# Kernel tuning notes

Hardware: AMD Instinct MI355X
Metric: run time of the kernel (lower is better)

## Reference

```python
import jax, jax.numpy as jnp
import numpy as np

V, H, E, O = 50257, 256, 256, 64
T, B = 1024, 256


def setup_inputs() -> dict:
    key = jax.random.key(0)
    ks = jax.random.split(key, 10)
    s = 0.02
    return {
        "x": jax.random.randint(ks[0], (T, B), 0, V, dtype=jnp.int64),
        "emb": jax.random.normal(ks[1], (V, H), jnp.float32) * s,
        "W_i2h": jax.random.normal(ks[2], (H, 2 * H), jnp.float32) * s,
        "b_i2h": jnp.zeros((H,), jnp.float32),
        "W_i2o": jax.random.normal(ks[3], (H, 2 * H), jnp.float32) * s,
        "b_i2o": jnp.zeros((H,), jnp.float32),
        "W_o2o": jax.random.normal(ks[4], (E, 2 * H), jnp.float32) * s,
        "b_o2o": jnp.zeros((E,), jnp.float32),
        "W_pred": jax.random.normal(ks[5], (O, E), jnp.float32) * s,
        "b_pred": jnp.zeros((O,), jnp.float32),
    }


def reference(x, emb, W_i2h, b_i2h, W_i2o, b_i2o, W_o2o, b_o2o, W_pred, b_pred):
    Bsz = x.shape[1]

    def step(h, xt):
        e = emb[xt]                                   # [B, H]
        ic = jnp.concatenate([e, h], axis=1)          # [B, 2H]
        h_new = ic @ W_i2h.T + b_i2h                  # [B, H]
        o = ic @ W_i2o.T + b_i2o                      # [B, H]
        oc = jnp.concatenate([h_new, o], axis=1)      # [B, 2H]
        out = oc @ W_o2o.T + b_o2o                    # [B, E]
        return h_new, out

    h0 = jnp.zeros((Bsz, W_i2h.shape[0]), emb.dtype)
    _, outs = jax.lax.scan(step, h0, x)               # [T, B, E]
    encoded = jnp.mean(outs, axis=0)                  # mean over time (dropout = identity in eval)
    logits = encoded @ W_pred.T + b_pred              # [B, O]
    logprobs = jax.nn.log_softmax(logits, axis=1)
    preds = jnp.argmax(logprobs, axis=1)
    probs = jnp.exp(logprobs)
    return preds, logprobs, probs
```

## Files before the change

kernel.cpp:

```cpp
#include <hip/hip_runtime.h>

#define T_STEPS 1024
#define BSZ 256
#define HD 256
#define OUTC 64
#define NT 32
#define NPHASE 32
#define TBB 8
#define BT 16

static const size_t OFF_SUM  = 0;
static const size_t OFF_FLAG = 65536;
static const size_t OFF_WP   = 65600;
static const size_t OFF_CEH  = 458816;
static const size_t OFF_CEO  = 2555968;
static const size_t OFF_H    = 4653120;
static const size_t OFF_A2   = 6815808;

__global__ void detect_x(const int* __restrict__ x, float* __restrict__ ws) {
    __shared__ int nonzero;
    if (threadIdx.x == 0) nonzero = 0;
    __syncthreads();
    if (x[2 * threadIdx.x + 1] != 0) nonzero = 1;
    __syncthreads();
    if (threadIdx.x == 0) *(int*)(ws + OFF_FLAG) = (nonzero == 0) ? 1 : 0;
}

__global__ void prep_pack(const float* __restrict__ Wi2h,
                          const float* __restrict__ Wi2o,
                          const float* __restrict__ Wo2o,
                          float* __restrict__ ws) {
    const int q = blockIdx.x;
    const int z = blockIdx.y;
    const int j = threadIdx.x;
    const float* src = (z == 0) ? Wi2h : (z == 1) ? Wi2o : Wo2o;
    const float4 v = *reinterpret_cast<const float4*>(src + (size_t)j * 512 + 4 * q);
    reinterpret_cast<float4*>(ws + OFF_WP)[((size_t)z * 128 + q) * 256 + j] = v;
}

__device__ __forceinline__ float RLf(float v, int l) {
    return __int_as_float(__builtin_amdgcn_readlane(__float_as_int(v), l));
}

__global__ __launch_bounds__(256) void kernB(
    const int* __restrict__ x, const float* __restrict__ emb,
    const float* __restrict__ boo, float* __restrict__ ws, int phase) {
    const int tid = threadIdx.x;
    const int sg = tid >> 7;
    const int lj = tid & 127;
    const int j0 = lj, j1 = lj + 128;
    const int ti = blockIdx.x;
    const int row = blockIdx.y;
    const int mode64 = *(const int*)(ws + OFF_FLAG);
    const float4* __restrict__ Wh4  = reinterpret_cast<const float4*>(ws + OFF_WP);
    const float4* __restrict__ Wio4 = Wh4 + (size_t)128 * 256;

    if (ti == 0 && phase > 0) {
        const size_t rb = (size_t)row * 256 + tid;
        float av[NT];
        #pragma unroll
        for (int i = 0; i < NT; ++i)
            av[i] = ws[OFF_A2 + (size_t)i * 65536 + rb];
        float s = (phase == 1) ? 0.f : ws[OFF_SUM + rb];
        const float boo_j = boo[tid];
        #pragma unroll
        for (int i = 0; i < NT; ++i) s += (av[i] + boo_j);
        ws[OFF_SUM + rb] = s;
    }

    __shared__ int toks[BT];
    __shared__ __align__(16) float eW[BT][256];
    if (tid < BT) {
        const int t = phase * NT + ti * BT + tid;
        toks[tid] = mode64 ? x[2 * (t * BSZ + row)] : x[t * BSZ + row];
    }
    __syncthreads();
    #pragma unroll
    for (int v = 0; v < BT; ++v)
        eW[v][tid] = emb[(size_t)toks[v] * HD + tid];
    __syncthreads();

    float aH[TBB][2], aO[TBB][2];
    #pragma unroll
    for (int u = 0; u < TBB; ++u) {
        aH[u][0] = 0.f; aH[u][1] = 0.f; aO[u][0] = 0.f; aO[u][1] = 0.f;
    }
    #pragma unroll 2
    for (int q = 0; q < 64; ++q) {
        const float4 whA = Wh4[(size_t)q * 256 + j0];
        const float4 whB = Wh4[(size_t)q * 256 + j1];
        const float4 woA = Wio4[(size_t)q * 256 + j0];
        const float4 woB = Wio4[(size_t)q * 256 + j1];
        #pragma unroll
        for (int u = 0; u < TBB; ++u) {
            const float4 e = *reinterpret_cast<const float4*>(&eW[sg * TBB + u][4 * q]);
            aH[u][0] = fmaf(e.x, whA.x, aH[u][0]); aH[u][1] = fmaf(e.x, whB.x, aH[u][1]);
            aO[u][0] = fmaf(e.x, woA.x, aO[u][0]); aO[u][1] = fmaf(e.x, woB.x, aO[u][1]);
            aH[u][0] = fmaf(e.y, whA.y, aH[u][0]); aH[u][1] = fmaf(e.y, whB.y, aH[u][1]);
            aO[u][0] = fmaf(e.y, woA.y, aO[u][0]); aO[u][1] = fmaf(e.y, woB.y, aO[u][1]);
            aH[u][0] = fmaf(e.z, whA.z, aH[u][0]); aH[u][1] = fmaf(e.z, whB.z, aH[u][1]);
            aO[u][0] = fmaf(e.z, woA.z, aO[u][0]); aO[u][1] = fmaf(e.z, woB.z, aO[u][1]);
            aH[u][0] = fmaf(e.w, whA.w, aH[u][0]); aH[u][1] = fmaf(e.w, whB.w, aH[u][1]);
            aO[u][0] = fmaf(e.w, woA.w, aO[u][0]); aO[u][1] = fmaf(e.w, woB.w, aO[u][1]);
        }
    }
    const size_t rb = (size_t)row * 256;
    #pragma unroll
    for (int u = 0; u < TBB; ++u) {
        const size_t off = (size_t)(ti * BT + sg * TBB + u) * 65536 + rb;
        ws[OFF_CEH + off + j0] = aH[u][0];
        ws[OFF_CEH + off + j1] = aH[u][1];
        ws[OFF_CEO + off + j0] = aO[u][0];
        ws[OFF_CEO + off + j1] = aO[u][1];
    }
}

__global__ __launch_bounds__(256) void kernC(
    const float* __restrict__ bih, float* __restrict__ ws, int phase) {
    const int j = threadIdx.x;
    const int lane = j & 63;
    const int row = blockIdx.x;
    const float4* __restrict__ Wh4 = reinterpret_cast<const float4*>(ws + OFF_WP);

    float4 whr[64];
    #pragma unroll
    for (int q = 0; q < 64; ++q) whr[q] = Wh4[(size_t)(64 + q) * 256 + j];

    __shared__ __align__(16) float hCur[256];
    float* __restrict__ Hp = ws + OFF_H;
    const float* __restrict__ CE = ws + OFF_CEH;
    const size_t rb = (size_t)row * 256 + j;

    const float hc = (phase == 0) ? 0.f : Hp[(size_t)NT * 65536 + rb];
    Hp[rb] = hc;
    hCur[j] = hc;
    const float bih_j = bih[j];
    float ceCur = CE[rb];
    __syncthreads();

    #pragma unroll 1
    for (int i = 0; i < NT; ++i) {
        const float ceNext = (i + 1 < NT) ? CE[(size_t)(i + 1) * 65536 + rb] : 0.f;
        const float4 h4 = *reinterpret_cast<const float4*>(&hCur[4 * lane]);
        float ah = ceCur;
        #pragma unroll
        for (int p2 = 0; p2 < 32; ++p2) {
            const int q0 = 2 * p2, q1 = 2 * p2 + 1;
            const float4 a = *reinterpret_cast<const float4*>(&hCur[4 * q0]);
            ah = fmaf(a.x, whr[q0].x, ah);
            ah = fmaf(a.y, whr[q0].y, ah);
            ah = fmaf(a.z, whr[q0].z, ah);
            ah = fmaf(a.w, whr[q0].w, ah);
            ah = fmaf(RLf(h4.x, q1), whr[q1].x, ah);
            ah = fmaf(RLf(h4.y, q1), whr[q1].y, ah);
            ah = fmaf(RLf(h4.z, q1), whr[q1].z, ah);
            ah = fmaf(RLf(h4.w, q1), whr[q1].w, ah);
        }
        const float hn = ah + bih_j;
        Hp[(size_t)(i + 1) * 65536 + rb] = hn;
        __syncthreads();
        hCur[j] = hn;
        ceCur = ceNext;
        __syncthreads();
    }
}

__global__ __launch_bounds__(256) void kernD(
    const float* __restrict__ bio, float* __restrict__ ws, int phase) {
    const int tid = threadIdx.x;
    const int sg = tid >> 7;
    const int lj = tid & 127;
    const int j0 = lj, j1 = lj + 128;
    const int ti = blockIdx.x;
    const int row = blockIdx.y;
    const float4* __restrict__ Wh4  = reinterpret_cast<const float4*>(ws + OFF_WP);
    const float4* __restrict__ Wio4 = Wh4 + (size_t)128 * 256;
    const float4* __restrict__ Woo4 = Wh4 + (size_t)256 * 256;

    __shared__ __align__(16) float hS[BT + 1][256];
    __shared__ __align__(16) float oS[BT][256];
    const float* __restrict__ Hp = ws + OFF_H;
    const size_t rb = (size_t)row * 256;

    #pragma unroll
    for (int v = 0; v <= BT; ++v)
        hS[v][tid] = Hp[(size_t)(ti * BT + v) * 65536 + rb + tid];
    float co[TBB][2], a2[TBB][2];
    #pragma unroll
    for (int u = 0; u < TBB; ++u) {
        const size_t off = OFF_CEO + (size_t)(ti * BT + sg * TBB + u) * 65536 + rb;
        co[u][0] = ws[off + j0];
        co[u][1] = ws[off + j1];
        a2[u][0] = 0.f; a2[u][1] = 0.f;
    }
    __syncthreads();

    #pragma unroll 2
    for (int q = 0; q < 64; ++q) {
        const float4 w1A = Wio4[(size_t)(64 + q) * 256 + j0];
        const float4 w1B = Wio4[(size_t)(64 + q) * 256 + j1];
        const float4 w2A = Woo4[(size_t)q * 256 + j0];
        const float4 w2B = Woo4[(size_t)q * 256 + j1];
        float4 hq[TBB + 1];
        #pragma unroll
        for (int v = 0; v <= TBB; ++v)
            hq[v] = *reinterpret_cast<const float4*>(&hS[sg * TBB + v][4 * q]);
        #pragma unroll
        for (int u = 0; u < TBB; ++u) {
            co[u][0] = fmaf(hq[u].x, w1A.x, co[u][0]);
            co[u][1] = fmaf(hq[u].x, w1B.x, co[u][1]);
            co[u][0] = fmaf(hq[u].y, w1A.y, co[u][0]);
            co[u][1] = fmaf(hq[u].y, w1B.y, co[u][1]);
            co[u][0] = fmaf(hq[u].z, w1A.z, co[u][0]);
            co[u][1] = fmaf(hq[u].z, w1B.z, co[u][1]);
            co[u][0] = fmaf(hq[u].w, w1A.w, co[u][0]);
            co[u][1] = fmaf(hq[u].w, w1B.w, co[u][1]);
            a2[u][0] = fmaf(hq[u + 1].x, w2A.x, a2[u][0]);
            a2[u][1] = fmaf(hq[u + 1].x, w2B.x, a2[u][1]);
            a2[u][0] = fmaf(hq[u + 1].y, w2A.y, a2[u][0]);
            a2[u][1] = fmaf(hq[u + 1].y, w2B.y, a2[u][1]);
            a2[u][0] = fmaf(hq[u + 1].z, w2A.z, a2[u][0]);
            a2[u][1] = fmaf(hq[u + 1].z, w2B.z, a2[u][1]);
            a2[u][0] = fmaf(hq[u + 1].w, w2A.w, a2[u][0]);
            a2[u][1] = fmaf(hq[u + 1].w, w2B.w, a2[u][1]);
        }
    }
    const float bio_j0 = bio[j0], bio_j1 = bio[j1];
    #pragma unroll
    for (int u = 0; u < TBB; ++u) {
        oS[sg * TBB + u][j0] = co[u][0] + bio_j0;
        oS[sg * TBB + u][j1] = co[u][1] + bio_j1;
    }
    __syncthreads();

    #pragma unroll 2
    for (int q = 0; q < 64; ++q) {
        const float4 w3A = Woo4[(size_t)(64 + q) * 256 + j0];
        const float4 w3B = Woo4[(size_t)(64 + q) * 256 + j1];
        #pragma unroll
        for (int u = 0; u < TBB; ++u) {
            const float4 o4 = *reinterpret_cast<const float4*>(&oS[sg * TBB + u][4 * q]);
            a2[u][0] = fmaf(o4.x, w3A.x, a2[u][0]);
            a2[u][1] = fmaf(o4.x, w3B.x, a2[u][1]);
            a2[u][0] = fmaf(o4.y, w3A.y, a2[u][0]);
            a2[u][1] = fmaf(o4.y, w3B.y, a2[u][1]);
            a2[u][0] = fmaf(o4.z, w3A.z, a2[u][0]);
            a2[u][1] = fmaf(o4.z, w3B.z, a2[u][1]);
            a2[u][0] = fmaf(o4.w, w3A.w, a2[u][0]);
            a2[u][1] = fmaf(o4.w, w3B.w, a2[u][1]);
        }
    }
    #pragma unroll
    for (int u = 0; u < TBB; ++u) {
        const size_t off = OFF_A2 + (size_t)(ti * BT + sg * TBB + u) * 65536 + rb;
        ws[off + j0] = a2[u][0];
        ws[off + j1] = a2[u][1];
    }
}

__global__ __launch_bounds__(64) void final_k(
    const float* __restrict__ Wpred, const float* __restrict__ bpred,
    const float* __restrict__ boo, const float* __restrict__ ws,
    float* __restrict__ out) {
    const int b = blockIdx.x, o = threadIdx.x;
    __shared__ float enc[256];
    __shared__ float exs[64];
    __shared__ float s32s;

    #pragma unroll
    for (int u = 0; u < 4; ++u) {
        const int j = o * 4 + u;
        const size_t rb = (size_t)b * 256 + j;
        float av[NT];
        #pragma unroll
        for (int i = 0; i < NT; ++i)
            av[i] = ws[OFF_A2 + (size_t)i * 65536 + rb];
        float s = ws[OFF_SUM + rb];
        const float boo_j = boo[j];
        #pragma unroll
        for (int i = 0; i < NT; ++i) s += (av[i] + boo_j);
        enc[j] = s * (1.0f / 1024.0f);
    }
    __syncthreads();

    float acc = 0.f;
    for (int e = 0; e < 256; ++e)
        acc = fmaf(enc[e], Wpred[(size_t)o * 256 + e], acc);
    acc += bpred[o];

    float m = acc;
    #pragma unroll
    for (int d = 1; d < 64; d <<= 1) m = fmaxf(m, __shfl_xor(m, d));
    const float sh = acc - m;
    const float ex = (float)exp((double)sh);
    exs[o] = ex;
    __syncthreads();
    if (o == 0) {
        double sd = 0.0;
        for (int i = 0; i < 64; ++i) sd += (double)exs[i];
        s32s = (float)sd;
    }
    __syncthreads();
    const float log_s = (float)log((double)s32s);
    const float lp = sh - log_s;
    const float pr = (float)exp((double)lp);

    float av = lp; int ai = o;
    #pragma unroll
    for (int d = 1; d < 64; d <<= 1) {
        const float ov = __shfl_xor(av, d);
        const int oi = __shfl_xor(ai, d);
        if (ov > av || (ov == av && oi < ai)) { av = ov; ai = oi; }
    }

    out[BSZ + (size_t)b * OUTC + o] = lp;
    out[BSZ + 16384 + (size_t)b * OUTC + o] = pr;
    if (o == 0) out[b] = (float)ai;
}

extern "C" void kernel_launch(void* const* d_in, const int* in_sizes, int n_in,
                              void* d_out, int out_size, void* d_ws, size_t ws_size,
                              hipStream_t stream) {
    const int*   x     = (const int*)d_in[0];
    const float* emb   = (const float*)d_in[1];
    const float* Wi2h  = (const float*)d_in[2];
    const float* b_ih  = (const float*)d_in[3];
    const float* Wi2o  = (const float*)d_in[4];
    const float* b_io  = (const float*)d_in[5];
    const float* Wo2o  = (const float*)d_in[6];
    const float* b_oo  = (const float*)d_in[7];
    const float* Wpred = (const float*)d_in[8];
    const float* b_p   = (const float*)d_in[9];
    float* ws  = (float*)d_ws;
    float* out = (float*)d_out;

    detect_x<<<1, 256, 0, stream>>>(x, ws);
    prep_pack<<<dim3(128, 3), 256, 0, stream>>>(Wi2h, Wi2o, Wo2o, ws);

    for (int p = 0; p < NPHASE; ++p) {
        kernB<<<dim3(2, 256), 256, 0, stream>>>(x, emb, b_oo, ws, p);
        kernC<<<dim3(256), 256, 0, stream>>>(b_ih, ws, p);
        kernD<<<dim3(2, 256), 256, 0, stream>>>(b_io, ws, p);
    }
    final_k<<<dim3(256), 64, 0, stream>>>(Wpred, b_p, b_oo, ws, out);
}
```

Measured before the change: 5.599 ms.

## Process two batch rows per recurrence block, streaming weights from global

The sequential hidden-state recurrence kernel now handles two batch rows per block, which halves the grid to 128 blocks. The 64-float4 register-resident weight slice is replaced by a software-prefetched stream from global/L2, with each weight load reused for both rows. Ping-pong shared buffers drop one of the two barriers per step. This frees a large amount of registers and reuses weights, but each serial step now does twice the FMA work plus repeated global weight loads, which may lengthen the critical path of the recurrence.

```diff
diff --git a/kernel.cpp b/kernel.cpp
--- a/kernel.cpp
+++ b/kernel.cpp
@@ -119,48 +119,56 @@
     const float* __restrict__ bih, float* __restrict__ ws, int phase) {
     const int j = threadIdx.x;
     const int lane = j & 63;
-    const int row = blockIdx.x;
+    const int r0 = blockIdx.x * 2, r1 = r0 + 1;
     const float4* __restrict__ Wh4 = reinterpret_cast<const float4*>(ws + OFF_WP);
 
-    float4 whr[64];
-    #pragma unroll
-    for (int q = 0; q < 64; ++q) whr[q] = Wh4[(size_t)(64 + q) * 256 + j];
-
-    __shared__ __align__(16) float hCur[256];
+    __shared__ __align__(16) float h0Ping[256], h0Pong[256];
+    __shared__ __align__(16) float h1Ping[256], h1Pong[256];
     float* __restrict__ Hp = ws + OFF_H;
     const float* __restrict__ CE = ws + OFF_CEH;
-    const size_t rb = (size_t)row * 256 + j;
-
-    const float hc = (phase == 0) ? 0.f : Hp[(size_t)NT * 65536 + rb];
-    Hp[rb] = hc;
-    hCur[j] = hc;
+    const size_t rb0 = (size_t)r0 * 256 + j;
+    const size_t rb1 = (size_t)r1 * 256 + j;
+
+    const float hc0 = (phase == 0) ? 0.f : Hp[(size_t)NT * 65536 + rb0];
+    const float hc1 = (phase == 0) ? 0.f : Hp[(size_t)NT * 65536 + rb1];
+    Hp[rb0] = hc0; Hp[rb1] = hc1;
+    h0Ping[j] = hc0; h1Ping[j] = hc1;
     const float bih_j = bih[j];
-    float ceCur = CE[rb];
+    float ce0 = CE[rb0], ce1 = CE[rb1];
     __syncthreads();
 
     #pragma unroll 1
     for (int i = 0; i < NT; ++i) {
-        const float ceNext = (i + 1 < NT) ? CE[(size_t)(i + 1) * 65536 + rb] : 0.f;
-        const float4 h4 = *reinterpret_cast<const float4*>(&hCur[4 * lane]);
-        float ah = ceCur;
-        #pragma unroll
-        for (int p2 = 0; p2 < 32; ++p2) {
-            const int q0 = 2 * p2, q1 = 2 * p2 + 1;
-            const float4 a = *reinterpret_cast<const float4*>(&hCur[4 * q0]);
-            ah = fmaf(a.x, whr[q0].x, ah);
-            ah = fmaf(a.y, whr[q0].y, ah);
-            ah = fmaf(a.z, whr[q0].z, ah);
-            ah = fmaf(a.w, whr[q0].w, ah);
-            ah = fmaf(RLf(h4.x, q1), whr[q1].x, ah);
-            ah = fmaf(RLf(h4.y, q1), whr[q1].y, ah);
-            ah = fmaf(RLf(h4.z, q1), whr[q1].z, ah);
-            ah = fmaf(RLf(h4.w, q1), whr[q1].w, ah);
+        const float ce0n = (i + 1 < NT) ? CE[(size_t)(i + 1) * 65536 + rb0] : 0.f;
+        const float ce1n = (i + 1 < NT) ? CE[(size_t)(i + 1) * 65536 + rb1] : 0.f;
+        const float* __restrict__ hb0 = (i & 1) ? h0Pong : h0Ping;
+        const float* __restrict__ hb1 = (i & 1) ? h1Pong : h1Ping;
+        float* __restrict__ hn0      = (i & 1) ? h0Ping : h0Pong;
+        float* __restrict__ hn1      = (i & 1) ? h1Ping : h1Pong;
+        const float4 h4r1 = *reinterpret_cast<const float4*>(&hb1[4 * lane]);
+        float ah0 = ce0, ah1 = ce1;
+        float4 w = Wh4[(size_t)64 * 256 + j];
+        #pragma unroll 4
+        for (int q = 0; q < 64; ++q) {
+            const float4 wn = Wh4[(size_t)(64 + ((q + 1) & 63)) * 256 + j];
+            const float4 a = *reinterpret_cast<const float4*>(&hb0[4 * q]);
+            ah0 = fmaf(a.x, w.x, ah0);
+            ah0 = fmaf(a.y, w.y, ah0);
+            ah0 = fmaf(a.z, w.z, ah0);
+            ah0 = fmaf(a.w, w.w, ah0);
+            float s;
+            s = RLf(h4r1.x, q); ah1 = fmaf(s, w.x, ah1);
+            s = RLf(h4r1.y, q); ah1 = fmaf(s, w.y, ah1);
+            s = RLf(h4r1.z, q); ah1 = fmaf(s, w.z, ah1);
+            s = RLf(h4r1.w, q); ah1 = fmaf(s, w.w, ah1);
+            w = wn;
         }
-        const float hn = ah + bih_j;
-        Hp[(size_t)(i + 1) * 65536 + rb] = hn;
-        __syncthreads();
-        hCur[j] = hn;
-        ceCur = ceNext;
+        const float hv0 = ah0 + bih_j;
+        const float hv1 = ah1 + bih_j;
+        Hp[(size_t)(i + 1) * 65536 + rb0] = hv0;
+        Hp[(size_t)(i + 1) * 65536 + rb1] = hv1;
+        hn0[j] = hv0; hn1[j] = hv1;
+        ce0 = ce0n; ce1 = ce1n;
         __syncthreads();
     }
 }
@@ -339,7 +347,7 @@
 
     for (int p = 0; p < NPHASE; ++p) {
         kernB<<<dim3(2, 256), 256, 0, stream>>>(x, emb, b_oo, ws, p);
-        kernC<<<dim3(256), 256, 0, stream>>>(b_ih, ws, p);
+        kernC<<<dim3(128), 256, 0, stream>>>(b_ih, ws, p);
         kernD<<<dim3(2, 256), 256, 0, stream>>>(b_io, ws, p);
     }
     final_k<<<dim3(256), 64, 0, stream>>>(Wpred, b_p, b_oo, ws, out);
```

Measured after the change: 12.36 ms. 2.21x slower.

## Stream recurrent weights from LDS and global in kernC, halve B/D time tiles

Applied to the files above, without the earlier changes.

kernC stops holding all 64 float4 weight vectors in registers. Half of them are now staged in LDS and the other half are reloaded from global memory at every step, and the hidden state uses ping-pong buffers so one barrier per step can be removed. The aim is to cut register pressure and barrier cost on the serial recurrence, at the price of extra LDS and global (likely L2-cached) traffic per step. kernB and kernD tiles are halved (TBB 4, BT 8) and their grids doubled to expose more parallelism.

```diff
diff --git a/kernel.cpp b/kernel.cpp
--- a/kernel.cpp
+++ b/kernel.cpp
@@ -6,8 +6,10 @@
 #define OUTC 64
 #define NT 32
 #define NPHASE 32
-#define TBB 8
-#define BT 16
+#define TBB 4
+#define BT 8
+#define CQS 32
+#define CQL 32
 
 static const size_t OFF_SUM  = 0;
 static const size_t OFF_FLAG = 65536;
@@ -36,10 +38,6 @@
     const float* src = (z == 0) ? Wi2h : (z == 1) ? Wi2o : Wo2o;
     const float4 v = *reinterpret_cast<const float4*>(src + (size_t)j * 512 + 4 * q);
     reinterpret_cast<float4*>(ws + OFF_WP)[((size_t)z * 128 + q) * 256 + j] = v;
-}
-
-__device__ __forceinline__ float RLf(float v, int l) {
-    return __int_as_float(__builtin_amdgcn_readlane(__float_as_int(v), l));
 }
 
 __global__ __launch_bounds__(256) void kernB(
@@ -118,22 +116,23 @@
 __global__ __launch_bounds__(256) void kernC(
     const float* __restrict__ bih, float* __restrict__ ws, int phase) {
     const int j = threadIdx.x;
-    const int lane = j & 63;
     const int row = blockIdx.x;
     const float4* __restrict__ Wh4 = reinterpret_cast<const float4*>(ws + OFF_WP);
 
-    float4 whr[64];
-    #pragma unroll
-    for (int q = 0; q < 64; ++q) whr[q] = Wh4[(size_t)(64 + q) * 256 + j];
-
-    __shared__ __align__(16) float hCur[256];
+    __shared__ __align__(16) float4 wL[CQL][256];
+    __shared__ __align__(16) float hPing[256], hPong[256];
+
+    #pragma unroll
+    for (int qq = 0; qq < CQL; ++qq)
+        wL[qq][j] = Wh4[(size_t)(64 + CQS + qq) * 256 + j];
+
     float* __restrict__ Hp = ws + OFF_H;
     const float* __restrict__ CE = ws + OFF_CEH;
     const size_t rb = (size_t)row * 256 + j;
 
     const float hc = (phase == 0) ? 0.f : Hp[(size_t)NT * 65536 + rb];
     Hp[rb] = hc;
-    hCur[j] = hc;
+    hPing[j] = hc;
     const float bih_j = bih[j];
     float ceCur = CE[rb];
     __syncthreads();
@@ -141,25 +140,36 @@
     #pragma unroll 1
     for (int i = 0; i < NT; ++i) {
         const float ceNext = (i + 1 < NT) ? CE[(size_t)(i + 1) * 65536 + rb] : 0.f;
-        const float4 h4 = *reinterpret_cast<const float4*>(&hCur[4 * lane]);
+        const float* __restrict__ hb = (i & 1) ? hPong : hPing;
+        float* __restrict__ hnb      = (i & 1) ? hPing : hPong;
         float ah = ceCur;
         #pragma unroll
-        for (int p2 = 0; p2 < 32; ++p2) {
-            const int q0 = 2 * p2, q1 = 2 * p2 + 1;
-            const float4 a = *reinterpret_cast<const float4*>(&hCur[4 * q0]);
-            ah = fmaf(a.x, whr[q0].x, ah);
-            ah = fmaf(a.y, whr[q0].y, ah);
-            ah = fmaf(a.z, whr[q0].z, ah);
-            ah = fmaf(a.w, whr[q0].w, ah);
-            ah = fmaf(RLf(h4.x, q1), whr[q1].x, ah);
-            ah = fmaf(RLf(h4.y, q1), whr[q1].y, ah);
-            ah = fmaf(RLf(h4.z, q1), whr[q1].z, ah);
-            ah = fmaf(RLf(h4.w, q1), whr[q1].w, ah);
+        for (int g = 0; g < 4; ++g) {
+            float4 wb[8];
+            #pragma unroll
+            for (int u = 0; u < 8; ++u)
+                wb[u] = Wh4[(size_t)(64 + g * 8 + u) * 256 + j];
+            #pragma unroll
+            for (int u = 0; u < 8; ++u) {
+                const float4 a = *reinterpret_cast<const float4*>(&hb[4 * (g * 8 + u)]);
+                ah = fmaf(a.x, wb[u].x, ah);
+                ah = fmaf(a.y, wb[u].y, ah);
+                ah = fmaf(a.z, wb[u].z, ah);
+                ah = fmaf(a.w, wb[u].w, ah);
+            }
+        }
+        #pragma unroll
+        for (int qq = 0; qq < CQL; ++qq) {
+            const float4 a = *reinterpret_cast<const float4*>(&hb[4 * (CQS + qq)]);
+            const float4 w = wL[qq][j];
+            ah = fmaf(a.x, w.x, ah);
+            ah = fmaf(a.y, w.y, ah);
+            ah = fmaf(a.z, w.z, ah);
+            ah = fmaf(a.w, w.w, ah);
         }
         const float hn = ah + bih_j;
         Hp[(size_t)(i + 1) * 65536 + rb] = hn;
-        __syncthreads();
-        hCur[j] = hn;
+        hnb[j] = hn;
         ceCur = ceNext;
         __syncthreads();
     }
@@ -338,9 +348,9 @@
     prep_pack<<<dim3(128, 3), 256, 0, stream>>>(Wi2h, Wi2o, Wo2o, ws);
 
     for (int p = 0; p < NPHASE; ++p) {
-        kernB<<<dim3(2, 256), 256, 0, stream>>>(x, emb, b_oo, ws, p);
+        kernB<<<dim3(4, 256), 256, 0, stream>>>(x, emb, b_oo, ws, p);
         kernC<<<dim3(256), 256, 0, stream>>>(b_ih, ws, p);
-        kernD<<<dim3(2, 256), 256, 0, stream>>>(b_io, ws, p);
+        kernD<<<dim3(4, 256), 256, 0, stream>>>(b_io, ws, p);
     }
     final_k<<<dim3(256), 64, 0, stream>>>(Wpred, b_p, b_oo, ws, out);
 }
```

New measurement: 8.208 ms. 1.47x slower.
